# Performance work log

Hardware: AMD Instinct MI355X
Metric: run time of the kernel (lower is better)

Reference implementation:

```python
import jax, jax.numpy as jnp
import numpy as np

THRESH = 0.7
MASK_WEIGHT = 0.7
IM_WEIGHT = 0.3
P = 2

B, C, H, W = 32, 8, 256, 256


def setup_inputs() -> dict:
    key = jax.random.key(0)
    k1, k2 = jax.random.split(key)
    output = jax.random.normal(k1, (B, C, H, W), dtype=jnp.float32)
    target = jax.random.uniform(k2, (B, C, H, W), dtype=jnp.float32)  # mask channel in [0,1] for BCE
    return {"output": output, "target": target}


def _bce_mean(p, t):
    # torch.nn.BCELoss clamps log terms at -100
    logp = jnp.clip(jnp.log(p), -100.0)
    log1mp = jnp.clip(jnp.log1p(-p), -100.0)
    return -jnp.mean(t * logp + (1.0 - t) * log1mp, axis=(0, 2, 3))  # mean over B,H,W -> [G]


def reference(output, target):
    b, c, h, w = output.shape
    g = c // 4
    out = output.reshape(b, g, 4, h, w)
    tar = target.reshape(b, g, 4, h, w)

    out_mask = jax.nn.sigmoid(out[:, :, 3])          # [B,G,H,W]
    tar_mask = tar[:, :, 3]
    mask_loss = _bce_mean(out_mask, tar_mask)        # [G]

    diff = out[:, :, :3] - jax.lax.stop_gradient(tar[:, :, :3])  # target_img.detach()
    if P == 2:
        diff_norm = jnp.sqrt(jnp.sum(diff * diff, axis=2))       # [B,G,H,W]
    else:
        diff_norm = jnp.sum(jnp.abs(diff) ** P, axis=2) ** (1.0 / P)

    masked = jnp.where(out_mask > THRESH, diff_norm, 0.0)        # [B,G,H,W]
    count = jnp.sum(masked != 0.0, axis=(2, 3)).astype(diff_norm.dtype)  # [B,G] nonzero count
    msum = jnp.sum(masked, axis=(2, 3))                          # [B,G]
    fallback = jnp.mean(diff_norm, axis=(2, 3))                  # [B,G]
    per_sample = jnp.where(count > 0, msum / jnp.maximum(count, 1.0), fallback)
    nocs_loss = jnp.mean(per_sample, axis=0)                     # [G] (sum over batch / batch_size)

    loss_per_group = MASK_WEIGHT * mask_loss + IM_WEIGHT * nocs_loss
    return jnp.mean(loss_per_group)  # TotalLoss / Den
```

## Files before the change

kernel.cpp:

```cpp
#include <hip/hip_runtime.h>

constexpr int   Bsz = 32, Csz = 8, Hsz = 256, Wsz = 256;
constexpr int   HW  = Hsz * Wsz;
constexpr int   G   = Csz / 4;
constexpr int   NBG = Bsz * G;
constexpr float MASK_WEIGHT = 0.7f;
constexpr float IM_WEIGHT   = 0.3f;
constexpr float XTHRESH = 0.8472978603872037f;

constexpr int BLK   = 256;
constexpr int ITERS = 2;
constexpr int PIX4_PER_BG   = HW / 4;
constexpr int BLOCKS_PER_BG = PIX4_PER_BG / (BLK * ITERS);
constexpr int NB = NBG * BLOCKS_PER_BG;

__device__ __forceinline__ float get(const float4& v, int e) {
    return e == 0 ? v.x : e == 1 ? v.y : e == 2 ? v.z : v.w;
}

__global__ __launch_bounds__(256) void lp_mask_main(
    const float* __restrict__ out, const float* __restrict__ tar,
    float* __restrict__ ws)
{
    const int tid   = threadIdx.x;
    const int blk   = blockIdx.x;
    const int bg    = blk / BLOCKS_PER_BG;
    const int chunk = blk % BLOCKS_PER_BG;

    const size_t base = (size_t)bg * 4 * HW;
    const float4* po = reinterpret_cast<const float4*>(out + base);
    const float4* pt = reinterpret_cast<const float4*>(tar + base);
    constexpr int P4 = HW / 4;

    float bce = 0.0f, msum = 0.0f, cnt = 0.0f, dsum = 0.0f;

    constexpr float LOG2E = 1.4426950408889634f;
    constexpr float LN2   = 0.6931471805599453f;

#pragma unroll
    for (int it = 0; it < ITERS; ++it) {
        const int idx = chunk * (BLK * ITERS) + it * BLK + tid;
        const float4 a0 = po[idx];
        const float4 a1 = po[idx + P4];
        const float4 a2 = po[idx + 2 * P4];
        const float4 a3 = po[idx + 3 * P4];
        const float4 b0 = pt[idx];
        const float4 b1 = pt[idx + P4];
        const float4 b2 = pt[idx + 2 * P4];
        const float4 b3 = pt[idx + 3 * P4];

#pragma unroll
        for (int e = 0; e < 4; ++e) {
            const float x  = get(a3, e);
            const float t  = get(b3, e);
            const float d0 = get(a0, e) - get(b0, e);
            const float d1 = get(a1, e) - get(b1, e);
            const float d2 = get(a2, e) - get(b2, e);

            const float ax = __builtin_fabsf(x);
            const float ex = __builtin_exp2f(-ax * LOG2E);
            const float sp = fmaxf(x, 0.0f) + __builtin_log2f(1.0f + ex) * LN2;
            bce += __builtin_fmaf(t, x, -sp);

            const float dn = __builtin_sqrtf(d0 * d0 + d1 * d1 + d2 * d2);
            dsum += dn;
            if (x > XTHRESH) {
                msum += dn;
                cnt  += (dn != 0.0f) ? 1.0f : 0.0f;
            }
        }
    }

#pragma unroll
    for (int off = 32; off > 0; off >>= 1) {
        bce  += __shfl_down(bce,  off, 64);
        msum += __shfl_down(msum, off, 64);
        cnt  += __shfl_down(cnt,  off, 64);
        dsum += __shfl_down(dsum, off, 64);
    }

    __shared__ float s[4][4];
    const int wave = tid >> 6, lane = tid & 63;
    if (lane == 0) {
        s[wave][0] = bce; s[wave][1] = msum; s[wave][2] = cnt; s[wave][3] = dsum;
    }
    __syncthreads();
    if (tid == 0) {
        float rb = 0.0f, rm = 0.0f, rc = 0.0f, rd = 0.0f;
#pragma unroll
        for (int w = 0; w < 4; ++w) {
            rb += s[w][0]; rm += s[w][1]; rc += s[w][2]; rd += s[w][3];
        }
        ws[blk]          = rb;
        ws[NB + blk]     = rm;
        ws[2 * NB + blk] = rc;
        ws[3 * NB + blk] = rd;
    }
}

__global__ __launch_bounds__(64) void lp_mask_final(
    const float* __restrict__ ws, float* __restrict__ outp)
{
    const int t = threadIdx.x;

    float b = 0.0f, m = 0.0f, c = 0.0f, d = 0.0f;
    for (int i = 0; i < BLOCKS_PER_BG; ++i) {
        const int blk = t * BLOCKS_PER_BG + i;
        b += ws[blk];
        m += ws[NB + blk];
        c += ws[2 * NB + blk];
        d += ws[3 * NB + blk];
    }

    float ps = (c > 0.0f) ? (m / fmaxf(c, 1.0f)) : (d / (float)HW);

#pragma unroll
    for (int off = 32; off > 0; off >>= 1) {
        ps += __shfl_down(ps, off, 64);
        b  += __shfl_down(b,  off, 64);
    }

    if (t == 0) {
        const float mask_mean = -b / ((float)G * (float)Bsz * (float)HW);
        const float nocs_mean = ps / (float)(Bsz * G);
        outp[0] = MASK_WEIGHT * mask_mean + IM_WEIGHT * nocs_mean;
    }
}

extern "C" void kernel_launch(void* const* d_in, const int* in_sizes, int n_in,
                              void* d_out, int out_size, void* d_ws, size_t ws_size,
                              hipStream_t stream) {
    const float* out = (const float*)d_in[0];
    const float* tar = (const float*)d_in[1];
    float* ws = (float*)d_ws;
    float* o  = (float*)d_out;

    lp_mask_main<<<NB, BLK, 0, stream>>>(out, tar, ws);
    lp_mask_final<<<1, 64, 0, stream>>>(ws, o);
}
```

Before: 146.4 us.

## Double-buffer loads across iterations and vectorize final reduction reads

Doubles the work per block (ITERS 2→4) and software-pipelines the global loads: the next iteration's eight float4 loads are issued into a second register buffer before the current one is computed. The final reduction kernel now reads workspace partials as float4 with an unrolled loop. The aim is to hide memory latency and reduce block count and partial-sum traffic, at the cost of higher register pressure and fewer blocks, which may lower occupancy.

After: 146.6 us. Within noise of the previous version (+0.1%).

```diff
diff --git a/kernel.cpp b/kernel.cpp
--- a/kernel.cpp
+++ b/kernel.cpp
@@ -9,10 +9,11 @@
 constexpr float XTHRESH = 0.8472978603872037f;
 
 constexpr int BLK   = 256;
-constexpr int ITERS = 2;
+constexpr int ITERS = 4;
 constexpr int PIX4_PER_BG   = HW / 4;
 constexpr int BLOCKS_PER_BG = PIX4_PER_BG / (BLK * ITERS);
 constexpr int NB = NBG * BLOCKS_PER_BG;
+
 
 __device__ __forceinline__ float get(const float4& v, int e) {
     return e == 0 ? v.x : e == 1 ? v.y : e == 2 ? v.z : v.w;
@@ -37,25 +38,36 @@
     constexpr float LOG2E = 1.4426950408889634f;
     constexpr float LN2   = 0.6931471805599453f;
 
+    const int idx0 = chunk * (BLK * ITERS) + tid;
+
+    float4 bufA[8], bufB[8];
+
+#define LD8(dst, idx)                                                   \
+    do {                                                                \
+        (dst)[0] = po[(idx)];            (dst)[1] = po[(idx) + P4];     \
+        (dst)[2] = po[(idx) + 2 * P4];   (dst)[3] = po[(idx) + 3 * P4]; \
+        (dst)[4] = pt[(idx)];            (dst)[5] = pt[(idx) + P4];     \
+        (dst)[6] = pt[(idx) + 2 * P4];   (dst)[7] = pt[(idx) + 3 * P4]; \
+    } while (0)
+
+    LD8(bufA, idx0);
+
 #pragma unroll
     for (int it = 0; it < ITERS; ++it) {
-        const int idx = chunk * (BLK * ITERS) + it * BLK + tid;
-        const float4 a0 = po[idx];
-        const float4 a1 = po[idx + P4];
-        const float4 a2 = po[idx + 2 * P4];
-        const float4 a3 = po[idx + 3 * P4];
-        const float4 b0 = pt[idx];
-        const float4 b1 = pt[idx + P4];
-        const float4 b2 = pt[idx + 2 * P4];
-        const float4 b3 = pt[idx + 3 * P4];
+        float4* C = (it & 1) ? bufB : bufA;
+        float4* N = (it & 1) ? bufA : bufB;
+        if (it + 1 < ITERS) {
+            const int idxn = idx0 + (it + 1) * BLK;
+            LD8(N, idxn);
+        }
 
 #pragma unroll
         for (int e = 0; e < 4; ++e) {
-            const float x  = get(a3, e);
-            const float t  = get(b3, e);
-            const float d0 = get(a0, e) - get(b0, e);
-            const float d1 = get(a1, e) - get(b1, e);
-            const float d2 = get(a2, e) - get(b2, e);
+            const float x  = get(C[3], e);
+            const float t  = get(C[7], e);
+            const float d0 = get(C[0], e) - get(C[4], e);
+            const float d1 = get(C[1], e) - get(C[5], e);
+            const float d2 = get(C[2], e) - get(C[6], e);
 
             const float ax = __builtin_fabsf(x);
             const float ex = __builtin_exp2f(-ax * LOG2E);
@@ -70,6 +82,7 @@
             }
         }
     }
+#undef LD8
 
 #pragma unroll
     for (int off = 32; off > 0; off >>= 1) {
@@ -102,14 +115,20 @@
     const float* __restrict__ ws, float* __restrict__ outp)
 {
     const int t = threadIdx.x;
+    constexpr int NPB = BLOCKS_PER_BG;
+    const float4* wb = reinterpret_cast<const float4*>(ws) + t * (NPB / 4);
+    const float4* wm = reinterpret_cast<const float4*>(ws + NB) + t * (NPB / 4);
+    const float4* wc = reinterpret_cast<const float4*>(ws + 2 * NB) + t * (NPB / 4);
+    const float4* wd = reinterpret_cast<const float4*>(ws + 3 * NB) + t * (NPB / 4);
 
     float b = 0.0f, m = 0.0f, c = 0.0f, d = 0.0f;
-    for (int i = 0; i < BLOCKS_PER_BG; ++i) {
-        const int blk = t * BLOCKS_PER_BG + i;
-        b += ws[blk];
-        m += ws[NB + blk];
-        c += ws[2 * NB + blk];
-        d += ws[3 * NB + blk];
+#pragma unroll
+    for (int i = 0; i < NPB / 4; ++i) {
+        const float4 vb = wb[i], vm = wm[i], vc = wc[i], vd = wd[i];
+        b += vb.x + vb.y + vb.z + vb.w;
+        m += vm.x + vm.y + vm.z + vm.w;
+        c += vc.x + vc.y + vc.z + vc.w;
+        d += vd.x + vd.y + vd.z + vd.w;
     }
 
     float ps = (c > 0.0f) ? (m / fmaxf(c, 1.0f)) : (d / (float)HW);
```
